# Performance work log

Measured on AMD Instinct MI355X. Metric: run time of the kernel, lower is better.

## Reference

```python
import jax, jax.numpy as jnp
import numpy as np

EPS = 1e-4  # ProtoPNet epsilon in distance-to-similarity transform


def setup_inputs() -> dict:
    key = jax.random.key(0)
    k1, k2, k3 = jax.random.split(key, 3)
    B, C, T = 128, 128, 777   # backbone feature map [B, C, T]
    P, NC = 500, 5            # prototypes, classes
    x = jax.random.normal(k1, (B, C, T), dtype=jnp.float32)
    prototypes = jax.random.uniform(k2, (P, C), dtype=jnp.float32)
    last_w = jax.random.normal(k3, (P, NC), dtype=jnp.float32)
    return {"x": x, "prototypes": prototypes, "last_w": last_w}


def reference(x, prototypes, last_w):
    # Prototype layer via the conv-trick L2 expansion:
    x2 = jnp.sum(x * x, axis=1)                      # [B, T]
    p2 = jnp.sum(prototypes * prototypes, axis=1)    # [P]
    xp = jnp.einsum('bct,pc->bpt', x, prototypes)    # [B, P, T]  (dominant GEMM)
    d = jnp.maximum(x2[:, None, :] - 2.0 * xp + p2[None, :, None], 0.0)  # [B, P, T]
    # Min-pool over all patches (global min over temporal axis)
    min_d = jnp.min(d, axis=2)                       # [B, P]
    # Distance -> similarity: log((d + 1) / (d + eps))
    sim = jnp.log((min_d + 1.0) / (min_d + EPS))     # [B, P]
    # Final evidence layer
    logits = sim @ last_w                            # [B, num_classes]
    return logits
```

## Files before the change

kernel.cpp:

```cpp
#include <hip/hip_runtime.h>
#include <hip/hip_bf16.h>

#define B_DIM 128
#define C_DIM 128
#define T_DIM 777
#define P_DIM 500
#define P_PAD 512
#define NCLS  5
#define EPSV  1e-4f
#define NT    25

typedef unsigned short u16;
typedef unsigned int   u32;
typedef __attribute__((ext_vector_type(8))) short short8;
typedef __attribute__((ext_vector_type(4))) float f32x4;
typedef float float4u __attribute__((ext_vector_type(4), aligned(4)));

__device__ __forceinline__ u16 f2bf(float f) {
    u32 u = __float_as_uint(f);
    u += 0x7FFFu + ((u >> 16) & 1u);
    return (u16)(u >> 16);
}

__global__ __launch_bounds__(256, 2) void fused_gemm_min(
    const float* __restrict__ x,
    const float* __restrict__ proto,
    float* __restrict__ wsmin) {

    const int o = blockIdx.x;
    const int xcd = o & 7, j = o >> 3;
    const int b   = xcd * 16 + (j >> 2);
    const int pt  = (j >> 1) & 1, th = j & 1;
    const int it0 = th ? 13 : 0;
    const int itN = th ? NT : 13;

    const int tid = threadIdx.x;
    const int w = tid >> 6, l = tid & 63;
    const int row16 = l & 15, kq = l >> 4;
    const int wp = pt * 256 + w * 64;

    const int c0  = (tid >> 3) << 2;
    const int tl0 = (tid & 7) << 2;

    __shared__ __align__(16) char  smem[32 * 256];
    __shared__ __align__(16) float x2p[4][32];

    const float* xb = x + (size_t)b * C_DIM * T_DIM;

    short8 afr[4][4];
#pragma unroll
    for (int ps = 0; ps < 4; ++ps) {
        const int r = wp + ps * 16 + row16;
#pragma unroll
        for (int kst = 0; kst < 4; ++kst) {
            const int k0 = kst * 32 + kq * 8;
            float f[8];
            if (r < P_DIM) {
                float4 u0 = *(const float4*)(proto + r * C_DIM + k0);
                float4 u1 = *(const float4*)(proto + r * C_DIM + k0 + 4);
                f[0]=u0.x; f[1]=u0.y; f[2]=u0.z; f[3]=u0.w;
                f[4]=u1.x; f[5]=u1.y; f[6]=u1.z; f[7]=u1.w;
            } else {
#pragma unroll
                for (int q = 0; q < 8; ++q) f[q] = 0.f;
            }
            short8 s8;
#pragma unroll
            for (int q = 0; q < 8; ++q) s8[q] = (short)f2bf(f[q]);
            afr[ps][kst] = s8;
        }
    }

    float vb[4][4];
    auto loadv = [&](int it) {
        const int tb = it * 32 + tl0;
        if (tb + 3 < T_DIM) {
#pragma unroll
            for (int r = 0; r < 4; ++r) {
                float4u u = *(const float4u*)(xb + (c0 + r) * T_DIM + tb);
                vb[r][0]=u[0]; vb[r][1]=u[1]; vb[r][2]=u[2]; vb[r][3]=u[3];
            }
        } else {
#pragma unroll
            for (int r = 0; r < 4; ++r)
#pragma unroll
                for (int jj = 0; jj < 4; ++jj) {
                    const int t = tb + jj;
                    vb[r][jj] = (t < T_DIM) ? xb[(c0 + r) * T_DIM + t] : 0.f;
                }
        }
    };

    loadv(it0);

    f32x4 minv[4];
#pragma unroll
    for (int ps = 0; ps < 4; ++ps) minv[ps] = (f32x4){1e30f, 1e30f, 1e30f, 1e30f};

    for (int it = it0; it < itN; ++it) {
        const int t0 = it * 32;

        float s[4];
#pragma unroll
        for (int jj = 0; jj < 4; ++jj)
            s[jj] = vb[0][jj]*vb[0][jj] + vb[1][jj]*vb[1][jj]
                  + vb[2][jj]*vb[2][jj] + vb[3][jj]*vb[3][jj];

#pragma unroll
        for (int jj = 0; jj < 4; ++jj) {
            const u32 lo = (u32)f2bf(vb[0][jj]) | ((u32)f2bf(vb[1][jj]) << 16);
            const u32 hi = (u32)f2bf(vb[2][jj]) | ((u32)f2bf(vb[3][jj]) << 16);
            const int tl  = tl0 + jj;
            const int off = tl * 256 + (((c0 >> 3) ^ (tl & 7)) << 4) + ((c0 & 4) << 1);
            *(uint2*)(smem + off) = make_uint2(lo, hi);
        }

#pragma unroll
        for (int m = 8; m <= 32; m <<= 1)
#pragma unroll
            for (int jj = 0; jj < 4; ++jj) s[jj] += __shfl_xor(s[jj], m);
        if ((l >> 3) == 0) {
            float4 o4;
            o4.x = (t0 + tl0 + 0 < T_DIM) ? s[0] : 1e30f;
            o4.y = (t0 + tl0 + 1 < T_DIM) ? s[1] : 1e30f;
            o4.z = (t0 + tl0 + 2 < T_DIM) ? s[2] : 1e30f;
            o4.w = (t0 + tl0 + 3 < T_DIM) ? s[3] : 1e30f;
            *(float4*)(&x2p[w][tl0]) = o4;
        }
        __syncthreads();

        if (it + 1 < itN) loadv(it + 1);

        f32x4 acc[4][2];
#pragma unroll
        for (int ps = 0; ps < 4; ++ps)
#pragma unroll
            for (int ts = 0; ts < 2; ++ts) acc[ps][ts] = (f32x4){0.f, 0.f, 0.f, 0.f};

#pragma unroll
        for (int kst = 0; kst < 4; ++kst) {
            short8 bfr[2];
#pragma unroll
            for (int ts = 0; ts < 2; ++ts) {
                const int tl = ts * 16 + row16;
                const int gr = (kst * 4 + kq) ^ (tl & 7);
                bfr[ts] = *(const short8*)(smem + tl * 256 + (gr << 4));
            }
#pragma unroll
            for (int ps = 0; ps < 4; ++ps)
#pragma unroll
                for (int ts = 0; ts < 2; ++ts)
                    acc[ps][ts] = __builtin_amdgcn_mfma_f32_16x16x32_bf16(
                        afr[ps][kst], bfr[ts], acc[ps][ts], 0, 0, 0);
        }

        const float x2v0 = x2p[0][row16]      + x2p[1][row16]      + x2p[2][row16]      + x2p[3][row16];
        const float x2v1 = x2p[0][16 + row16] + x2p[1][16 + row16] + x2p[2][16 + row16] + x2p[3][16 + row16];
#pragma unroll
        for (int ps = 0; ps < 4; ++ps)
#pragma unroll
            for (int q = 0; q < 4; ++q) {
                minv[ps][q] = fminf(minv[ps][q], fmaf(-2.f, acc[ps][0][q], x2v0));
                minv[ps][q] = fminf(minv[ps][q], fmaf(-2.f, acc[ps][1][q], x2v1));
            }
        __syncthreads();
    }

#pragma unroll
    for (int m = 1; m <= 8; m <<= 1)
#pragma unroll
        for (int ps = 0; ps < 4; ++ps)
#pragma unroll
            for (int q = 0; q < 4; ++q)
                minv[ps][q] = fminf(minv[ps][q], __shfl_xor(minv[ps][q], m));

    if (row16 == 0) {
#pragma unroll
        for (int ps = 0; ps < 4; ++ps)
#pragma unroll
            for (int q = 0; q < 4; ++q) {
                const int p = wp + ps * 16 + kq * 4 + q;
                if (p < P_DIM)
                    wsmin[((size_t)b * P_PAD + p) * 2 + th] = minv[ps][q];
            }
    }
}

__global__ __launch_bounds__(256) void combine_logits(
    const float* __restrict__ proto, const float* __restrict__ lw,
    const float* __restrict__ wsmin, float* __restrict__ out) {
    const int b = blockIdx.x, tid = threadIdx.x;
    float a[NCLS] = {0.f, 0.f, 0.f, 0.f, 0.f};
    for (int p = tid; p < P_DIM; p += 256) {
        const float4* pr = (const float4*)(proto + p * C_DIM);
        float p2 = 0.f;
#pragma unroll
        for (int i = 0; i < 32; ++i) {
            float4 u = pr[i];
            p2 += u.x*u.x + u.y*u.y + u.z*u.z + u.w*u.w;
        }
        const size_t base = ((size_t)b * P_PAD + p) * 2;
        const float m  = fminf(wsmin[base], wsmin[base + 1]);
        const float md = fmaxf(m + p2, 0.f);
        const float sim = logf((md + 1.f) / (md + EPSV));
#pragma unroll
        for (int n = 0; n < NCLS; ++n) a[n] = fmaf(sim, lw[p * NCLS + n], a[n]);
    }
#pragma unroll
    for (int m = 1; m <= 32; m <<= 1)
#pragma unroll
        for (int n = 0; n < NCLS; ++n) a[n] += __shfl_xor(a[n], m);
    __shared__ float red[4][NCLS];
    const int w = tid >> 6, l = tid & 63;
    if (l == 0) {
#pragma unroll
        for (int n = 0; n < NCLS; ++n) red[w][n] = a[n];
    }
    __syncthreads();
    if (tid < NCLS)
        out[b * NCLS + tid] = red[0][tid] + red[1][tid] + red[2][tid] + red[3][tid];
}

__global__ __launch_bounds__(256) void fallback_k(const float* __restrict__ x,
                                                  const float* __restrict__ proto,
                                                  const float* __restrict__ lw,
                                                  float* __restrict__ out) {
    __shared__ float x2s[T_DIM];
    __shared__ float sims[P_DIM];
    int b = blockIdx.x, tid = threadIdx.x;
    for (int t = tid; t < T_DIM; t += 256) {
        float a = 0.f;
        for (int c = 0; c < C_DIM; ++c) { float v = x[((size_t)b * C_DIM + c) * T_DIM + t]; a = fmaf(v, v, a); }
        x2s[t] = a;
    }
    __syncthreads();
    for (int p = tid; p < P_DIM; p += 256) {
        float p2 = 0.f;
        for (int c = 0; c < C_DIM; ++c) { float v = proto[p * C_DIM + c]; p2 = fmaf(v, v, p2); }
        float mind = 1e30f;
        for (int t = 0; t < T_DIM; ++t) {
            float xp = 0.f;
            for (int c = 0; c < C_DIM; ++c)
                xp = fmaf(x[((size_t)b * C_DIM + c) * T_DIM + t], proto[p * C_DIM + c], xp);
            float d = fmaxf(x2s[t] - 2.f * xp + p2, 0.f);
            mind = fminf(mind, d);
        }
        sims[p] = logf((mind + 1.f) / (mind + EPSV));
    }
    __syncthreads();
    if (tid < NCLS) {
        float a = 0.f;
        for (int p = 0; p < P_DIM; ++p) a = fmaf(sims[p], lw[p * NCLS + tid], a);
        out[b * NCLS + tid] = a;
    }
}

extern "C" void kernel_launch(void* const* d_in, const int* in_sizes, int n_in,
                              void* d_out, int out_size, void* d_ws, size_t ws_size,
                              hipStream_t stream) {
    const float* x     = (const float*)d_in[0];
    const float* proto = (const float*)d_in[1];
    const float* lw    = (const float*)d_in[2];
    float* out = (float*)d_out;

    const size_t need = (size_t)B_DIM * P_PAD * 2 * sizeof(float);

    if (ws_size >= need) {
        float* wsmin = (float*)d_ws;
        fused_gemm_min<<<dim3(512), 256, 0, stream>>>(x, proto, wsmin);
        combine_logits<<<dim3(B_DIM), 256, 0, stream>>>(proto, lw, wsmin, out);
    } else {
        fallback_k<<<dim3(B_DIM), 256, 0, stream>>>(x, proto, lw, out);
    }
}
```

Baseline: 43.15 us.

## Double-buffer LDS tiles, split T three ways, use hardware bf16 packing

The time axis is now split into three chunks instead of two, giving 768 blocks, and launch bounds are raised to three blocks per CU. The LDS tile and x² partials are double-buffered, so the next tile is written after the MFMA work and each iteration needs only one barrier. Software bf16 rounding is replaced by the v_cvt_pk_bf16_f32 instruction, MFMA sections are wrapped in s_setprio, and partial minima are stored as float4 in a [th][b][p] workspace layout. The risks are register pressure at three blocks per CU and extra per-block prologue cost, since each block reloads its prototype fragments.

Measured after the change: 50.77 us. 1.18x slower.

```diff
diff --git a/kernel.cpp b/kernel.cpp
--- a/kernel.cpp
+++ b/kernel.cpp
@@ -16,23 +16,26 @@
 typedef __attribute__((ext_vector_type(4))) float f32x4;
 typedef float float4u __attribute__((ext_vector_type(4), aligned(4)));
 
-__device__ __forceinline__ u16 f2bf(float f) {
-    u32 u = __float_as_uint(f);
-    u += 0x7FFFu + ((u >> 16) & 1u);
-    return (u16)(u >> 16);
-}
-
-__global__ __launch_bounds__(256, 2) void fused_gemm_min(
+__device__ __forceinline__ u32 cvt_pk_bf16(float a, float b) {
+    u32 r;
+    asm("v_cvt_pk_bf16_f32 %0, %1, %2" : "=v"(r) : "v"(a), "v"(b));
+    return r;
+}
+
+__global__ __launch_bounds__(256, 3) void fused_gemm_min(
     const float* __restrict__ x,
     const float* __restrict__ proto,
     float* __restrict__ wsmin) {
 
-    const int o = blockIdx.x;
+    const int o   = blockIdx.x;
     const int xcd = o & 7, j = o >> 3;
-    const int b   = xcd * 16 + (j >> 2);
-    const int pt  = (j >> 1) & 1, th = j & 1;
-    const int it0 = th ? 13 : 0;
-    const int itN = th ? NT : 13;
+    const int bl  = j / 6;
+    const int r6  = j - bl * 6;
+    const int b   = xcd * 16 + bl;
+    const int pt  = r6 & 1;
+    const int th  = r6 >> 1;
+    const int it0 = (th == 0) ? 0 : (th == 1 ? 9 : 17);
+    const int itN = (th == 0) ? 9 : (th == 1 ? 17 : NT);
 
     const int tid = threadIdx.x;
     const int w = tid >> 6, l = tid & 63;
@@ -42,8 +45,8 @@
     const int c0  = (tid >> 3) << 2;
     const int tl0 = (tid & 7) << 2;
 
-    __shared__ __align__(16) char  smem[32 * 256];
-    __shared__ __align__(16) float x2p[4][32];
+    __shared__ __align__(16) char  smem[2][32 * 256];
+    __shared__ __align__(16) float x2p[2][4][32];
 
     const float* xb = x + (size_t)b * C_DIM * T_DIM;
 
@@ -54,20 +57,18 @@
 #pragma unroll
         for (int kst = 0; kst < 4; ++kst) {
             const int k0 = kst * 32 + kq * 8;
-            float f[8];
+            union { short8 s; u32 d[4]; } t;
             if (r < P_DIM) {
                 float4 u0 = *(const float4*)(proto + r * C_DIM + k0);
                 float4 u1 = *(const float4*)(proto + r * C_DIM + k0 + 4);
-                f[0]=u0.x; f[1]=u0.y; f[2]=u0.z; f[3]=u0.w;
-                f[4]=u1.x; f[5]=u1.y; f[6]=u1.z; f[7]=u1.w;
+                t.d[0] = cvt_pk_bf16(u0.x, u0.y);
+                t.d[1] = cvt_pk_bf16(u0.z, u0.w);
+                t.d[2] = cvt_pk_bf16(u1.x, u1.y);
+                t.d[3] = cvt_pk_bf16(u1.z, u1.w);
             } else {
-#pragma unroll
-                for (int q = 0; q < 8; ++q) f[q] = 0.f;
-            }
-            short8 s8;
-#pragma unroll
-            for (int q = 0; q < 8; ++q) s8[q] = (short)f2bf(f[q]);
-            afr[ps][kst] = s8;
+                t.d[0] = t.d[1] = t.d[2] = t.d[3] = 0u;
+            }
+            afr[ps][kst] = t.s;
         }
     }
 
@@ -91,30 +92,21 @@
         }
     };
 
-    loadv(it0);
-
-    f32x4 minv[4];
-#pragma unroll
-    for (int ps = 0; ps < 4; ++ps) minv[ps] = (f32x4){1e30f, 1e30f, 1e30f, 1e30f};
-
-    for (int it = it0; it < itN; ++it) {
+    auto write_tile = [&](int it, int bsel) {
         const int t0 = it * 32;
-
         float s[4];
 #pragma unroll
         for (int jj = 0; jj < 4; ++jj)
             s[jj] = vb[0][jj]*vb[0][jj] + vb[1][jj]*vb[1][jj]
                   + vb[2][jj]*vb[2][jj] + vb[3][jj]*vb[3][jj];
-
 #pragma unroll
         for (int jj = 0; jj < 4; ++jj) {
-            const u32 lo = (u32)f2bf(vb[0][jj]) | ((u32)f2bf(vb[1][jj]) << 16);
-            const u32 hi = (u32)f2bf(vb[2][jj]) | ((u32)f2bf(vb[3][jj]) << 16);
+            const u32 lo = cvt_pk_bf16(vb[0][jj], vb[1][jj]);
+            const u32 hi = cvt_pk_bf16(vb[2][jj], vb[3][jj]);
             const int tl  = tl0 + jj;
             const int off = tl * 256 + (((c0 >> 3) ^ (tl & 7)) << 4) + ((c0 & 4) << 1);
-            *(uint2*)(smem + off) = make_uint2(lo, hi);
-        }
-
+            *(uint2*)(smem[bsel] + off) = make_uint2(lo, hi);
+        }
 #pragma unroll
         for (int m = 8; m <= 32; m <<= 1)
 #pragma unroll
@@ -125,11 +117,22 @@
             o4.y = (t0 + tl0 + 1 < T_DIM) ? s[1] : 1e30f;
             o4.z = (t0 + tl0 + 2 < T_DIM) ? s[2] : 1e30f;
             o4.w = (t0 + tl0 + 3 < T_DIM) ? s[3] : 1e30f;
-            *(float4*)(&x2p[w][tl0]) = o4;
-        }
-        __syncthreads();
-
-        if (it + 1 < itN) loadv(it + 1);
+            *(float4*)(&x2p[bsel][w][tl0]) = o4;
+        }
+    };
+
+    f32x4 minv[4];
+#pragma unroll
+    for (int ps = 0; ps < 4; ++ps) minv[ps] = (f32x4){1e30f, 1e30f, 1e30f, 1e30f};
+
+    loadv(it0);
+    write_tile(it0, 0);
+    __syncthreads();
+
+    int cur = 0;
+    for (int it = it0; it < itN; ++it) {
+        const bool more = (it + 1 < itN);
+        if (more) loadv(it + 1);
 
         f32x4 acc[4][2];
 #pragma unroll
@@ -137,6 +140,8 @@
 #pragma unroll
             for (int ts = 0; ts < 2; ++ts) acc[ps][ts] = (f32x4){0.f, 0.f, 0.f, 0.f};
 
+        const char* sbase = smem[cur];
+        __builtin_amdgcn_s_setprio(1);
 #pragma unroll
         for (int kst = 0; kst < 4; ++kst) {
             short8 bfr[2];
@@ -144,7 +149,7 @@
             for (int ts = 0; ts < 2; ++ts) {
                 const int tl = ts * 16 + row16;
                 const int gr = (kst * 4 + kq) ^ (tl & 7);
-                bfr[ts] = *(const short8*)(smem + tl * 256 + (gr << 4));
+                bfr[ts] = *(const short8*)(sbase + tl * 256 + (gr << 4));
             }
 #pragma unroll
             for (int ps = 0; ps < 4; ++ps)
@@ -153,9 +158,12 @@
                     acc[ps][ts] = __builtin_amdgcn_mfma_f32_16x16x32_bf16(
                         afr[ps][kst], bfr[ts], acc[ps][ts], 0, 0, 0);
         }
-
-        const float x2v0 = x2p[0][row16]      + x2p[1][row16]      + x2p[2][row16]      + x2p[3][row16];
-        const float x2v1 = x2p[0][16 + row16] + x2p[1][16 + row16] + x2p[2][16 + row16] + x2p[3][16 + row16];
+        __builtin_amdgcn_s_setprio(0);
+
+        const float x2v0 = x2p[cur][0][row16]      + x2p[cur][1][row16]
+                         + x2p[cur][2][row16]      + x2p[cur][3][row16];
+        const float x2v1 = x2p[cur][0][16 + row16] + x2p[cur][1][16 + row16]
+                         + x2p[cur][2][16 + row16] + x2p[cur][3][16 + row16];
 #pragma unroll
         for (int ps = 0; ps < 4; ++ps)
 #pragma unroll
@@ -163,7 +171,10 @@
                 minv[ps][q] = fminf(minv[ps][q], fmaf(-2.f, acc[ps][0][q], x2v0));
                 minv[ps][q] = fminf(minv[ps][q], fmaf(-2.f, acc[ps][1][q], x2v1));
             }
+
+        if (more) write_tile(it + 1, cur ^ 1);
         __syncthreads();
+        cur ^= 1;
     }
 
 #pragma unroll
@@ -176,13 +187,11 @@
 
     if (row16 == 0) {
 #pragma unroll
-        for (int ps = 0; ps < 4; ++ps)
-#pragma unroll
-            for (int q = 0; q < 4; ++q) {
-                const int p = wp + ps * 16 + kq * 4 + q;
-                if (p < P_DIM)
-                    wsmin[((size_t)b * P_PAD + p) * 2 + th] = minv[ps][q];
-            }
+        for (int ps = 0; ps < 4; ++ps) {
+            const int p = wp + ps * 16 + kq * 4;
+            *(float4*)(&wsmin[((size_t)th * B_DIM + b) * P_PAD + p]) =
+                make_float4(minv[ps][0], minv[ps][1], minv[ps][2], minv[ps][3]);
+        }
     }
 }
 
@@ -199,8 +208,10 @@
             float4 u = pr[i];
             p2 += u.x*u.x + u.y*u.y + u.z*u.z + u.w*u.w;
         }
-        const size_t base = ((size_t)b * P_PAD + p) * 2;
-        const float m  = fminf(wsmin[base], wsmin[base + 1]);
+        const float m0 = wsmin[(0 * B_DIM + b) * P_PAD + p];
+        const float m1 = wsmin[(1 * B_DIM + b) * P_PAD + p];
+        const float m2 = wsmin[(2 * B_DIM + b) * P_PAD + p];
+        const float m  = fminf(fminf(m0, m1), m2);
         const float md = fmaxf(m + p2, 0.f);
         const float sim = logf((md + 1.f) / (md + EPSV));
 #pragma unroll
@@ -263,11 +274,11 @@
     const float* lw    = (const float*)d_in[2];
     float* out = (float*)d_out;
 
-    const size_t need = (size_t)B_DIM * P_PAD * 2 * sizeof(float);
+    const size_t need = (size_t)3 * B_DIM * P_PAD * sizeof(float);
 
     if (ws_size >= need) {
         float* wsmin = (float*)d_ws;
-        fused_gemm_min<<<dim3(512), 256, 0, stream>>>(x, proto, wsmin);
+        fused_gemm_min<<<dim3(768), 256, 0, stream>>>(x, proto, wsmin);
         combine_logits<<<dim3(B_DIM), 256, 0, stream>>>(proto, lw, wsmin, out);
     } else {
         fallback_k<<<dim3(B_DIM), 256, 0, stream>>>(x, proto, lw, out);
```
